# Performance work log

Hardware: AMD Instinct MI355X
Metric: run time of the kernel (lower is better)

## Reference

```python
import jax, jax.numpy as jnp
import numpy as np

N, E = 50000, 800000
IN, HID, HEADS, LAT = 128, 64, 4, 32
NEG_SLOPE = 0.2  # PyG GATv2Conv default negative_slope


def _glorot(key, shape):
    fan_in, fan_out = shape[0], shape[-1]
    lim = (6.0 / (fan_in + fan_out)) ** 0.5
    return jax.random.uniform(key, shape, jnp.float32, -lim, lim)


def setup_inputs() -> dict:
    keys = jax.random.split(jax.random.key(0), 10)
    x = jax.random.normal(keys[0], (N, IN), jnp.float32)
    edge_index = jax.random.randint(keys[1], (2, E), 0, N, jnp.int32)
    return {
        "x": x,
        "edge_index": edge_index,
        # layer 1: in -> hidden, heads=HEADS, concat=True
        "W_l1": _glorot(keys[2], (IN, HEADS * HID)),
        "W_r1": _glorot(keys[3], (IN, HEADS * HID)),
        "att1": _glorot(keys[4], (HEADS, HID)),
        "bias1": jnp.zeros((HEADS * HID,), jnp.float32),
        # layer 2: heads*hidden -> latent, heads=1, concat=False
        "W_l2": _glorot(keys[5], (HEADS * HID, LAT)),
        "W_r2": _glorot(keys[6], (HEADS * HID, LAT)),
        "att2": _glorot(keys[7], (1, LAT)),
        "bias2": jnp.zeros((LAT,), jnp.float32),
    }


def gatv2_layer(x, src, dst, W_l, W_r, att, bias, heads, out_ch, concat):
    """PyG GATv2Conv (eval mode, add_self_loops already applied to src/dst)."""
    n = x.shape[0]
    xl = (x @ W_l).reshape(n, heads, out_ch)  # source transform (messages)
    xr = (x @ W_r).reshape(n, heads, out_ch)  # target transform
    # per-edge attention logits: a^T LeakyReLU(xl[j] + xr[i])
    e = jax.nn.leaky_relu(xl[src] + xr[dst], NEG_SLOPE)  # [E, H, C]
    score = jnp.einsum('ehc,hc->eh', e, att)             # [E, H]
    # segment softmax over incoming edges of each dst node
    smax = jax.ops.segment_max(score, dst, num_segments=n)   # [N, H]
    ex = jnp.exp(score - smax[dst])
    denom = jax.ops.segment_sum(ex, dst, num_segments=n)     # [N, H]
    alpha = ex / denom[dst]                                  # [E, H]
    # scatter-add weighted source features
    out = jax.ops.segment_sum(xl[src] * alpha[..., None], dst, num_segments=n)
    out = out.reshape(n, heads * out_ch) if concat else out.mean(axis=1)
    return out + bias


def reference(x, edge_index, W_l1, W_r1, att1, bias1, W_l2, W_r2, att2, bias2):
    n = x.shape[0]
    # GATv2Conv adds self loops by default
    loops = jnp.arange(n, dtype=edge_index.dtype)
    src = jnp.concatenate([edge_index[0], loops])
    dst = jnp.concatenate([edge_index[1], loops])
    h = jax.nn.elu(gatv2_layer(x, src, dst, W_l1, W_r1, att1, bias1, HEADS, HID, True))
    z = gatv2_layer(h, src, dst, W_l2, W_r2, att2, bias2, 1, LAT, False)
    # decode: sigmoid(<z[row], z[col]>) over the original edges
    row, col = edge_index[0], edge_index[1]
    pred = jax.nn.sigmoid(jnp.sum(z[row] * z[col], axis=1))
    return pred
```

## Files before the change

kernel.cpp:

```cpp
#include <hip/hip_runtime.h>
#include <hip/hip_fp16.h>
#include <math.h>

#define N_NODES 50000
#define N_EDGES 800000
#define EP (N_EDGES + N_NODES)
#define IN_CH 128
#define HID 64
#define HEADS 4
#define F1 (HEADS * HID)
#define LAT 32
#define NEG 0.2f
#define CAP 64
#define NW (512 * 128 + 64 * 256)
#define ZQ 412502

typedef __attribute__((ext_vector_type(8))) short short8;
typedef __attribute__((ext_vector_type(8))) unsigned short ushort8v;
typedef __attribute__((ext_vector_type(4))) float f32x4;

__device__ __forceinline__ unsigned short f2bf(float f) {
    unsigned int x = __float_as_uint(f);
    x += 0x7fffu + ((x >> 16) & 1u);
    return (unsigned short)(x >> 16);
}
__device__ __forceinline__ float bf2f(unsigned short u) {
    return __uint_as_float(((unsigned int)u) << 16);
}
__device__ __forceinline__ float h2f(unsigned short u) {
    return __half2float(__ushort_as_half(u));
}
__device__ __forceinline__ f32x4 mfma_bf16(short8 a, short8 b, f32x4 c) {
    return __builtin_amdgcn_mfma_f32_16x16x32_bf16(a, b, c, 0, 0, 0);
}

__global__ void conv_w_zero(const float* __restrict__ Wl1, const float* __restrict__ Wr1,
                            const float* __restrict__ Wl2, const float* __restrict__ Wr2,
                            unsigned short* __restrict__ Wt1, unsigned short* __restrict__ Wt2,
                            int4* __restrict__ zbase) {
    int idx = blockIdx.x * 256 + threadIdx.x;
    if (idx < ZQ) zbase[idx] = make_int4(0, 0, 0, 0);
    if (idx < 512 * 128) {
        int n = idx >> 7, k = idx & 127;
        float v = (n < 256) ? Wl1[(size_t)k * 256 + n] : Wr1[(size_t)k * 256 + (n - 256)];
        Wt1[idx] = f2bf(v);
    } else if (idx < NW) {
        int j = idx - 512 * 128;
        int n = j >> 8, k = j & 255;
        float v = (n < 32) ? Wl2[(size_t)k * 32 + n] : Wr2[(size_t)k * 32 + (n - 32)];
        Wt2[j] = f2bf(v);
    }
}

__global__ __launch_bounds__(256) void gemm1_mfma(const float* __restrict__ x,
                                                  const unsigned short* __restrict__ Wt1,
                                                  unsigned short* __restrict__ xlh,
                                                  unsigned short* __restrict__ xrh) {
    int wave = threadIdx.x >> 6;
    int lane = threadIdx.x & 63;
    int quad = lane >> 4, lo = lane & 15;
    int row0 = blockIdx.x * 32;
    int colw = wave * 128;
    int rB0 = min(row0 + lo, N_NODES - 1);
    int rB1 = min(row0 + 16 + lo, N_NODES - 1);
    f32x4 acc[2][8];
#pragma unroll
    for (int rt = 0; rt < 2; rt++)
#pragma unroll
        for (int ct = 0; ct < 8; ct++) acc[rt][ct] = (f32x4){0.f, 0.f, 0.f, 0.f};
#pragma unroll
    for (int ks = 0; ks < 4; ks++) {
        int koff = ks * 32 + quad * 8;
        float4 fa0 = *(const float4*)(x + (size_t)rB0 * IN_CH + koff);
        float4 fb0 = *(const float4*)(x + (size_t)rB0 * IN_CH + koff + 4);
        float4 fa1 = *(const float4*)(x + (size_t)rB1 * IN_CH + koff);
        float4 fb1 = *(const float4*)(x + (size_t)rB1 * IN_CH + koff + 4);
        short8 b0, b1;
        b0[0] = f2bf(fa0.x); b0[1] = f2bf(fa0.y); b0[2] = f2bf(fa0.z); b0[3] = f2bf(fa0.w);
        b0[4] = f2bf(fb0.x); b0[5] = f2bf(fb0.y); b0[6] = f2bf(fb0.z); b0[7] = f2bf(fb0.w);
        b1[0] = f2bf(fa1.x); b1[1] = f2bf(fa1.y); b1[2] = f2bf(fa1.z); b1[3] = f2bf(fa1.w);
        b1[4] = f2bf(fb1.x); b1[5] = f2bf(fb1.y); b1[6] = f2bf(fb1.z); b1[7] = f2bf(fb1.w);
#pragma unroll
        for (int ct = 0; ct < 8; ct++) {
            short8 a = *(const short8*)(Wt1 + (size_t)(colw + ct * 16 + lo) * IN_CH + koff);
            acc[0][ct] = mfma_bf16(a, b0, acc[0][ct]);
            acc[1][ct] = mfma_bf16(a, b1, acc[1][ct]);
        }
    }
#pragma unroll
    for (int rt = 0; rt < 2; rt++) {
        int node = row0 + rt * 16 + lo;
        if (node < N_NODES) {
#pragma unroll
            for (int ct = 0; ct < 8; ct++) {
                int feat = colw + ct * 16 + quad * 4;
                ushort4 u;
                u.x = f2bf(acc[rt][ct][0]); u.y = f2bf(acc[rt][ct][1]);
                u.z = f2bf(acc[rt][ct][2]); u.w = f2bf(acc[rt][ct][3]);
                if (feat < F1)
                    *(ushort4*)(xlh + (size_t)node * F1 + feat) = u;
                else
                    *(ushort4*)(xrh + (size_t)node * F1 + (feat - F1)) = u;
            }
        }
    }
}

__global__ void scatter_bucket(const int* __restrict__ ei, int* __restrict__ cnt,
                               unsigned short* __restrict__ srcsP) {
    long e = (long)blockIdx.x * 256 + threadIdx.x;
    if (e >= EP) return;
    int s, d;
    if (e < N_EDGES) { s = ei[e]; d = ei[N_EDGES + e]; }
    else             { s = d = (int)(e - N_EDGES); }
    int pos = atomicAdd(&cnt[d], 1);
    if (pos < CAP) __builtin_nontemporal_store((unsigned short)s, &srcsP[(d << 6) + pos]);
}

__global__ __launch_bounds__(256) void fused_l1(const unsigned short* __restrict__ xlh,
                                                const unsigned short* __restrict__ xrh,
                                                unsigned short* __restrict__ hbf,
                                                const unsigned short* __restrict__ srcsP,
                                                const int* __restrict__ cnt,
                                                const float* __restrict__ att,
                                                const float* __restrict__ bias) {
    int wave = threadIdx.x >> 6;
    int lane = threadIdx.x & 63;
    int h = lane >> 5;
    int c = lane & 31;
    int c0 = c << 3;
    int d = blockIdx.x * 4 + wave;
    if (d >= N_NODES) return;
    ushort8v xru = *(const ushort8v*)(xrh + (size_t)d * F1 + c0);
    float4 atA = *(const float4*)(att + c0);
    float4 atB = *(const float4*)(att + c0 + 4);
    float xr8[8], at8[8] = {atA.x, atA.y, atA.z, atA.w, atB.x, atB.y, atB.z, atB.w};
    float a6[8], a4[8];
#pragma unroll
    for (int i = 0; i < 8; i++) {
        xr8[i] = bf2f(xru[i]);
        a6[i] = 0.6f * at8[i];
        a4[i] = 0.4f * at8[i];
    }
    int start = d << 6;
    int dg    = min(CAP, __builtin_amdgcn_readfirstlane(cnt[d]));
    float l = 0.f;
    float acc[8] = {};
    int jj = h;
    int s = srcsP[start + jj];
    ushort8v raw = *(const ushort8v*)(xlh + (size_t)s * F1 + c0);
    int sN = srcsP[start + jj + 2];
    int iters = (dg + 1) >> 1;
    for (int k = 0; k < iters; k++) {
        ushort8v cr = raw;
        raw = *(const ushort8v*)(xlh + (size_t)sN * F1 + c0);
        sN = srcsP[start + jj + 4];
        float a[8];
#pragma unroll
        for (int i = 0; i < 8; i++) a[i] = bf2f(cr[i]);
        float sc = 0.f;
#pragma unroll
        for (int i = 0; i < 8; i++) {
            float v = a[i] + xr8[i];
            sc = fmaf(v, a6[i], sc);
            sc = fmaf(fabsf(v), a4[i], sc);
        }
        sc += __shfl_xor(sc, 1);
        sc += __shfl_xor(sc, 2);
        sc += __shfl_xor(sc, 4);
        float ex = (jj < dg) ? __expf(sc) : 0.f;
        l += ex;
#pragma unroll
        for (int i = 0; i < 8; i++) acc[i] = fmaf(ex, a[i], acc[i]);
        jj += 2;
    }
    l += __shfl_xor(l, 32);
#pragma unroll
    for (int i = 0; i < 8; i++) acc[i] += __shfl_xor(acc[i], 32);
    if (h == 0) {
        float inv = 1.0f / l;
        float4 bA = *(const float4*)(bias + c0);
        float4 bB = *(const float4*)(bias + c0 + 4);
        float b8[8] = {bA.x, bA.y, bA.z, bA.w, bB.x, bB.y, bB.z, bB.w};
        ushort8v ho;
#pragma unroll
        for (int i = 0; i < 8; i++) {
            float o = acc[i] * inv + b8[i];
            o = o > 0.f ? o : __expf(o) - 1.0f;
            ho[i] = (unsigned short)f2bf(o);
        }
        *(ushort8v*)(hbf + (size_t)d * F1 + c0) = ho;
    }
}

__global__ __launch_bounds__(256) void gemm2_mfma(const unsigned short* __restrict__ hbf,
                                                  const unsigned short* __restrict__ Wt2,
                                                  __half* __restrict__ xl2h,
                                                  float* __restrict__ xr2) {
    int wave = threadIdx.x >> 6;
    int lane = threadIdx.x & 63;
    int quad = lane >> 4, lo = lane & 15;
    int row0 = blockIdx.x * 64 + wave * 16;
    int rB = min(row0 + lo, N_NODES - 1);
    f32x4 acc[4];
#pragma unroll
    for (int ct = 0; ct < 4; ct++) acc[ct] = (f32x4){0.f, 0.f, 0.f, 0.f};
#pragma unroll
    for (int ks = 0; ks < 8; ks++) {
        int koff = ks * 32 + quad * 8;
        short8 b = *(const short8*)(hbf + (size_t)rB * F1 + koff);
#pragma unroll
        for (int ct = 0; ct < 4; ct++) {
            short8 a = *(const short8*)(Wt2 + (size_t)(ct * 16 + lo) * F1 + koff);
            acc[ct] = mfma_bf16(a, b, acc[ct]);
        }
    }
    int node = row0 + lo;
    if (node < N_NODES) {
#pragma unroll
        for (int ct = 0; ct < 4; ct++) {
            int feat = ct * 16 + quad * 4;
            if (feat < LAT) {
                ushort4 u;
                u.x = __half_as_ushort(__float2half_rn(acc[ct][0]));
                u.y = __half_as_ushort(__float2half_rn(acc[ct][1]));
                u.z = __half_as_ushort(__float2half_rn(acc[ct][2]));
                u.w = __half_as_ushort(__float2half_rn(acc[ct][3]));
                *(ushort4*)((unsigned short*)xl2h + (size_t)node * LAT + feat) = u;
            } else {
                float4 f = make_float4(acc[ct][0], acc[ct][1], acc[ct][2], acc[ct][3]);
                *(float4*)(xr2 + (size_t)node * LAT + (feat - LAT)) = f;
            }
        }
    }
}

__global__ __launch_bounds__(256) void fused_l2(const __half* __restrict__ xl2h,
                                                const float* __restrict__ xr2,
                                                const unsigned short* __restrict__ srcsP,
                                                const int* __restrict__ cnt,
                                                const float* __restrict__ att,
                                                const float* __restrict__ bias,
                                                __half* __restrict__ zh) {
    int wave = threadIdx.x >> 6;
    int lane = threadIdx.x & 63;
    int q = lane >> 4;
    int c = lane & 15;
    int c2 = c << 1;
    int d = blockIdx.x * 4 + wave;
    if (d >= N_NODES) return;
    float xr0 = xr2[(size_t)d * LAT + c2];
    float xr1v = xr2[(size_t)d * LAT + c2 + 1];
    float av0 = att[c2], av1 = att[c2 + 1];
    float a60 = 0.6f * av0, a40 = 0.4f * av0;
    float a61 = 0.6f * av1, a41 = 0.4f * av1;
    int start = d << 6;
    int dg    = min(CAP, __builtin_amdgcn_readfirstlane(cnt[d]));
    float l = 0.f, acc0 = 0.f, acc1 = 0.f;
    int jj = q;
    int s = srcsP[start + jj];
    __half2 raw = *(const __half2*)(xl2h + (size_t)s * LAT + c2);
    int sN = srcsP[start + jj + 4];
    int iters = (dg + 3) >> 2;
    for (int k = 0; k < iters; k++) {
        __half2 cr = raw;
        raw = *(const __half2*)(xl2h + (size_t)sN * LAT + c2);
        sN = srcsP[start + jj + 8];
        float a0 = __half2float(cr.x), a1 = __half2float(cr.y);
        float v0 = a0 + xr0;
        float v1 = a1 + xr1v;
        float sc = 0.f;
        sc = fmaf(v0, a60, sc);
        sc = fmaf(fabsf(v0), a40, sc);
        sc = fmaf(v1, a61, sc);
        sc = fmaf(fabsf(v1), a41, sc);
        sc += __shfl_xor(sc, 1);
        sc += __shfl_xor(sc, 2);
        sc += __shfl_xor(sc, 4);
        sc += __shfl_xor(sc, 8);
        float ex = (jj < dg) ? __expf(sc) : 0.f;
        l += ex;
        acc0 = fmaf(ex, a0, acc0);
        acc1 = fmaf(ex, a1, acc1);
        jj += 4;
    }
    l += __shfl_xor(l, 16); acc0 += __shfl_xor(acc0, 16); acc1 += __shfl_xor(acc1, 16);
    l += __shfl_xor(l, 32); acc0 += __shfl_xor(acc0, 32); acc1 += __shfl_xor(acc1, 32);
    if (q == 0) {
        __half2 o;
        o.x = __float2half_rn(acc0 / l + bias[c2]);
        o.y = __float2half_rn(acc1 / l + bias[c2 + 1]);
        *(__half2*)(zh + (size_t)d * LAT + c2) = o;
    }
}

__global__ __launch_bounds__(256) void decode(const __half* __restrict__ zh,
                                              const int* __restrict__ ei,
                                              float* __restrict__ out) {
    int g = threadIdx.x >> 2;
    int lane = threadIdx.x & 3;
    long e = (long)blockIdx.x * 64 + g;
    if (e >= N_EDGES) return;
    int r = ei[e], c = ei[N_EDGES + e];
    int cc = lane << 3;
    ushort8v ur = *(const ushort8v*)((const unsigned short*)zh + (size_t)r * LAT + cc);
    ushort8v uc = *(const ushort8v*)((const unsigned short*)zh + (size_t)c * LAT + cc);
    float v = 0.f;
#pragma unroll
    for (int i = 0; i < 8; i++) {
        v += h2f(ur[i]) * h2f(uc[i]);
    }
    v += __shfl_xor(v, 1);
    v += __shfl_xor(v, 2);
    if (lane == 0) out[e] = 1.0f / (1.0f + __expf(-v));
}

extern "C" void kernel_launch(void* const* d_in, const int* in_sizes, int n_in,
                              void* d_out, int out_size, void* d_ws, size_t ws_size,
                              hipStream_t stream) {
    const float* x    = (const float*)d_in[0];
    const int*   ei   = (const int*)d_in[1];
    const float* Wl1  = (const float*)d_in[2];
    const float* Wr1  = (const float*)d_in[3];
    const float* att1 = (const float*)d_in[4];
    const float* b1   = (const float*)d_in[5];
    const float* Wl2  = (const float*)d_in[6];
    const float* Wr2  = (const float*)d_in[7];
    const float* att2 = (const float*)d_in[8];
    const float* b2   = (const float*)d_in[9];
    float* out = (float*)d_out;

    unsigned short* xrh = (unsigned short*)d_ws;
    unsigned short* hbf = xrh + (size_t)N_NODES * F1;
    unsigned short* xlh = hbf + (size_t)N_NODES * F1;
    int* cnt = (int*)(xlh + (size_t)N_NODES * F1);
    unsigned short* srcsP = (unsigned short*)(cnt + N_NODES);
    unsigned short* Wt1 = srcsP + (size_t)N_NODES * CAP + 16;
    unsigned short* Wt2 = Wt1 + 512 * 128;
    __half* xl2h = (__half*)xlh;
    float*  xr2  = (float*)(xl2h + (size_t)N_NODES * LAT);
    __half* zh   = (__half*)(xr2 + (size_t)N_NODES * LAT);

    conv_w_zero<<<(ZQ + 255) / 256, 256, 0, stream>>>(Wl1, Wr1, Wl2, Wr2, Wt1, Wt2,
                                                      (int4*)cnt);

    scatter_bucket<<<(EP + 255) / 256, 256, 0, stream>>>(ei, cnt, srcsP);

    gemm1_mfma<<<(N_NODES + 31) / 32, 256, 0, stream>>>(x, Wt1, xlh, xrh);

    fused_l1<<<(N_NODES + 3) / 4, 256, 0, stream>>>(xlh, xrh, hbf, srcsP, cnt, att1, b1);

    gemm2_mfma<<<(N_NODES + 63) / 64, 256, 0, stream>>>(hbf, Wt2, xl2h, xr2);
    fused_l2<<<(N_NODES + 3) / 4, 256, 0, stream>>>(xl2h, xr2, srcsP, cnt, att2, b2, zh);

    decode<<<(N_EDGES + 63) / 64, 256, 0, stream>>>(zh, ei, out);
}
```

Baseline: 324.7 us.

## Use packed bf16 convert, grid-stride fused_l1, and deepen gather prefetch

New measurement: 374.1 us. 1.15x slower.

```diff
diff --git a/kernel.cpp b/kernel.cpp
--- a/kernel.cpp
+++ b/kernel.cpp
@@ -14,10 +14,12 @@
 #define CAP 64
 #define NW (512 * 128 + 64 * 256)
 #define ZQ 412502
+#define L1_BLOCKS 2048
 
 typedef __attribute__((ext_vector_type(8))) short short8;
 typedef __attribute__((ext_vector_type(8))) unsigned short ushort8v;
 typedef __attribute__((ext_vector_type(4))) float f32x4;
+typedef __attribute__((ext_vector_type(4))) unsigned int uint4v;
 
 __device__ __forceinline__ unsigned short f2bf(float f) {
     unsigned int x = __float_as_uint(f);
@@ -32,6 +34,19 @@
 }
 __device__ __forceinline__ f32x4 mfma_bf16(short8 a, short8 b, f32x4 c) {
     return __builtin_amdgcn_mfma_f32_16x16x32_bf16(a, b, c, 0, 0, 0);
+}
+__device__ __forceinline__ unsigned cvt_pk_bf16(float lo, float hi) {
+    unsigned r;
+    asm("v_cvt_pk_bf16_f32 %0, %1, %2" : "=v"(r) : "v"(lo), "v"(hi));
+    return r;
+}
+__device__ __forceinline__ short8 pack_bf16x8(float4 A, float4 B) {
+    uint4v u;
+    u[0] = cvt_pk_bf16(A.x, A.y);
+    u[1] = cvt_pk_bf16(A.z, A.w);
+    u[2] = cvt_pk_bf16(B.x, B.y);
+    u[3] = cvt_pk_bf16(B.z, B.w);
+    return __builtin_bit_cast(short8, u);
 }
 
 __global__ void conv_w_zero(const float* __restrict__ Wl1, const float* __restrict__ Wr1,
@@ -75,11 +90,8 @@
         float4 fb0 = *(const float4*)(x + (size_t)rB0 * IN_CH + koff + 4);
         float4 fa1 = *(const float4*)(x + (size_t)rB1 * IN_CH + koff);
         float4 fb1 = *(const float4*)(x + (size_t)rB1 * IN_CH + koff + 4);
-        short8 b0, b1;
-        b0[0] = f2bf(fa0.x); b0[1] = f2bf(fa0.y); b0[2] = f2bf(fa0.z); b0[3] = f2bf(fa0.w);
-        b0[4] = f2bf(fb0.x); b0[5] = f2bf(fb0.y); b0[6] = f2bf(fb0.z); b0[7] = f2bf(fb0.w);
-        b1[0] = f2bf(fa1.x); b1[1] = f2bf(fa1.y); b1[2] = f2bf(fa1.z); b1[3] = f2bf(fa1.w);
-        b1[4] = f2bf(fb1.x); b1[5] = f2bf(fb1.y); b1[6] = f2bf(fb1.z); b1[7] = f2bf(fb1.w);
+        short8 b0 = pack_bf16x8(fa0, fb0);
+        short8 b1 = pack_bf16x8(fa1, fb1);
 #pragma unroll
         for (int ct = 0; ct < 8; ct++) {
             short8 a = *(const short8*)(Wt1 + (size_t)(colw + ct * 16 + lo) * IN_CH + koff);
@@ -94,13 +106,13 @@
 #pragma unroll
             for (int ct = 0; ct < 8; ct++) {
                 int feat = colw + ct * 16 + quad * 4;
-                ushort4 u;
-                u.x = f2bf(acc[rt][ct][0]); u.y = f2bf(acc[rt][ct][1]);
-                u.z = f2bf(acc[rt][ct][2]); u.w = f2bf(acc[rt][ct][3]);
+                uint2 u;
+                u.x = cvt_pk_bf16(acc[rt][ct][0], acc[rt][ct][1]);
+                u.y = cvt_pk_bf16(acc[rt][ct][2], acc[rt][ct][3]);
                 if (feat < F1)
-                    *(ushort4*)(xlh + (size_t)node * F1 + feat) = u;
+                    *(uint2*)(xlh + (size_t)node * F1 + feat) = u;
                 else
-                    *(ushort4*)(xrh + (size_t)node * F1 + (feat - F1)) = u;
+                    *(uint2*)(xrh + (size_t)node * F1 + (feat - F1)) = u;
             }
         }
     }
@@ -129,67 +141,73 @@
     int h = lane >> 5;
     int c = lane & 31;
     int c0 = c << 3;
-    int d = blockIdx.x * 4 + wave;
-    if (d >= N_NODES) return;
-    ushort8v xru = *(const ushort8v*)(xrh + (size_t)d * F1 + c0);
     float4 atA = *(const float4*)(att + c0);
     float4 atB = *(const float4*)(att + c0 + 4);
-    float xr8[8], at8[8] = {atA.x, atA.y, atA.z, atA.w, atB.x, atB.y, atB.z, atB.w};
+    float at8[8] = {atA.x, atA.y, atA.z, atA.w, atB.x, atB.y, atB.z, atB.w};
     float a6[8], a4[8];
 #pragma unroll
     for (int i = 0; i < 8; i++) {
-        xr8[i] = bf2f(xru[i]);
         a6[i] = 0.6f * at8[i];
         a4[i] = 0.4f * at8[i];
     }
-    int start = d << 6;
-    int dg    = min(CAP, __builtin_amdgcn_readfirstlane(cnt[d]));
-    float l = 0.f;
-    float acc[8] = {};
-    int jj = h;
-    int s = srcsP[start + jj];
-    ushort8v raw = *(const ushort8v*)(xlh + (size_t)s * F1 + c0);
-    int sN = srcsP[start + jj + 2];
-    int iters = (dg + 1) >> 1;
-    for (int k = 0; k < iters; k++) {
-        ushort8v cr = raw;
-        raw = *(const ushort8v*)(xlh + (size_t)sN * F1 + c0);
-        sN = srcsP[start + jj + 4];
-        float a[8];
-#pragma unroll
-        for (int i = 0; i < 8; i++) a[i] = bf2f(cr[i]);
-        float sc = 0.f;
-#pragma unroll
-        for (int i = 0; i < 8; i++) {
-            float v = a[i] + xr8[i];
-            sc = fmaf(v, a6[i], sc);
-            sc = fmaf(fabsf(v), a4[i], sc);
-        }
-        sc += __shfl_xor(sc, 1);
-        sc += __shfl_xor(sc, 2);
-        sc += __shfl_xor(sc, 4);
-        float ex = (jj < dg) ? __expf(sc) : 0.f;
-        l += ex;
-#pragma unroll
-        for (int i = 0; i < 8; i++) acc[i] = fmaf(ex, a[i], acc[i]);
-        jj += 2;
-    }
-    l += __shfl_xor(l, 32);
-#pragma unroll
-    for (int i = 0; i < 8; i++) acc[i] += __shfl_xor(acc[i], 32);
-    if (h == 0) {
-        float inv = 1.0f / l;
-        float4 bA = *(const float4*)(bias + c0);
-        float4 bB = *(const float4*)(bias + c0 + 4);
-        float b8[8] = {bA.x, bA.y, bA.z, bA.w, bB.x, bB.y, bB.z, bB.w};
-        ushort8v ho;
-#pragma unroll
-        for (int i = 0; i < 8; i++) {
-            float o = acc[i] * inv + b8[i];
-            o = o > 0.f ? o : __expf(o) - 1.0f;
-            ho[i] = (unsigned short)f2bf(o);
-        }
-        *(ushort8v*)(hbf + (size_t)d * F1 + c0) = ho;
+    float4 bA = *(const float4*)(bias + c0);
+    float4 bB = *(const float4*)(bias + c0 + 4);
+    float b8[8] = {bA.x, bA.y, bA.z, bA.w, bB.x, bB.y, bB.z, bB.w};
+
+    for (int d = blockIdx.x * 4 + wave; d < N_NODES; d += L1_BLOCKS * 4) {
+        ushort8v xru = *(const ushort8v*)(xrh + (size_t)d * F1 + c0);
+        float xr8[8];
+#pragma unroll
+        for (int i = 0; i < 8; i++) xr8[i] = bf2f(xru[i]);
+        int start = d << 6;
+        int dg    = min(CAP, __builtin_amdgcn_readfirstlane(cnt[d]));
+        float l = 0.f;
+        float acc[8] = {};
+        int jj = h;
+        int s0 = srcsP[start + jj];
+        int s1 = srcsP[start + jj + 2];
+        ushort8v rawA = *(const ushort8v*)(xlh + (size_t)s0 * F1 + c0);
+        ushort8v rawB = *(const ushort8v*)(xlh + (size_t)s1 * F1 + c0);
+        int sN = srcsP[start + jj + 4];
+        int iters = (dg + 1) >> 1;
+        for (int k = 0; k < iters; k++) {
+            ushort8v cr = rawA;
+            rawA = rawB;
+            rawB = *(const ushort8v*)(xlh + (size_t)sN * F1 + c0);
+            sN = srcsP[start + jj + 6];
+            float a[8];
+#pragma unroll
+            for (int i = 0; i < 8; i++) a[i] = bf2f(cr[i]);
+            float sc = 0.f;
+#pragma unroll
+            for (int i = 0; i < 8; i++) {
+                float v = a[i] + xr8[i];
+                sc = fmaf(v, a6[i], sc);
+                sc = fmaf(fabsf(v), a4[i], sc);
+            }
+            sc += __shfl_xor(sc, 1);
+            sc += __shfl_xor(sc, 2);
+            sc += __shfl_xor(sc, 4);
+            float ex = (jj < dg) ? __expf(sc) : 0.f;
+            l += ex;
+#pragma unroll
+            for (int i = 0; i < 8; i++) acc[i] = fmaf(ex, a[i], acc[i]);
+            jj += 2;
+        }
+        l += __shfl_xor(l, 32);
+#pragma unroll
+        for (int i = 0; i < 8; i++) acc[i] += __shfl_xor(acc[i], 32);
+        if (h == 0) {
+            float inv = 1.0f / l;
+            ushort8v ho;
+#pragma unroll
+            for (int i = 0; i < 8; i++) {
+                float o = acc[i] * inv + b8[i];
+                o = o > 0.f ? o : __expf(o) - 1.0f;
+                ho[i] = (unsigned short)f2bf(o);
+            }
+            *(ushort8v*)(hbf + (size_t)d * F1 + c0) = ho;
+        }
     }
 }
 
@@ -348,7 +366,7 @@
 
     gemm1_mfma<<<(N_NODES + 31) / 32, 256, 0, stream>>>(x, Wt1, xlh, xrh);
 
-    fused_l1<<<(N_NODES + 3) / 4, 256, 0, stream>>>(xlh, xrh, hbf, srcsP, cnt, att1, b1);
+    fused_l1<<<L1_BLOCKS, 256, 0, stream>>>(xlh, xrh, hbf, srcsP, cnt, att1, b1);
 
     gemm2_mfma<<<(N_NODES + 63) / 64, 256, 0, stream>>>(hbf, Wt2, xl2h, xr2);
     fused_l2<<<(N_NODES + 3) / 4, 256, 0, stream>>>(xl2h, xr2, srcsP, cnt, att2, b2, zh);
```
